# Kernel tuning notes

Measured on AMD Instinct MI355X. Metric: run time of the kernel, lower is better.

## Reference

```python
import jax, jax.numpy as jnp
import numpy as np

EPS = 1e-3  # keras LayerNormalization default epsilon


def _layernorm(y, gamma, beta):
    m = jnp.mean(y, axis=-1, keepdims=True)
    v = jnp.var(y, axis=-1, keepdims=True)
    return (y - m) * jax.lax.rsqrt(v + EPS) * gamma + beta


def setup_inputs() -> dict:
    key = jax.random.key(0)
    ks = jax.random.split(key, 3)
    B, S, D, F = 4, 8192, 512, 2048
    x = jax.random.normal(ks[0], (B, S, D), dtype=jnp.float32)
    W1 = jax.random.normal(ks[1], (D, F), dtype=jnp.float32) * (1.0 / np.sqrt(D))
    b1 = jnp.zeros((F,), dtype=jnp.float32)
    W2 = jax.random.normal(ks[2], (F, D), dtype=jnp.float32) * (1.0 / np.sqrt(F))
    b2 = jnp.zeros((D,), dtype=jnp.float32)
    g1 = jnp.ones((D,), dtype=jnp.float32)
    be1 = jnp.zeros((D,), dtype=jnp.float32)
    g2 = jnp.ones((D,), dtype=jnp.float32)
    be2 = jnp.zeros((D,), dtype=jnp.float32)
    return {"x": x, "W1": W1, "b1": b1, "W2": W2, "b2": b2,
            "g1": g1, "be1": be1, "g2": g2, "be2": be2}


def reference(x, W1, b1, W2, b2, g1, be1, g2, be2):
    # 2D FFT over (seq, embed) axes; keep real part (FNet mixing)
    fft = jnp.real(jnp.fft.fft2(x.astype(jnp.complex64), axes=(-2, -1)))
    proj_input = _layernorm(x + fft, g1, be1)
    # FFN: Dense(dense_dim, relu) -> Dense(embed_dim)
    h = jax.nn.relu(jnp.einsum('bsd,df->bsf', proj_input, W1) + b1)
    proj_output = jnp.einsum('bsf,fd->bsd', h, W2) + b2
    return _layernorm(proj_input + proj_output, g2, be2)
```

## Files before the change

kernel.cpp:

```cpp
#include <hip/hip_runtime.h>

typedef unsigned short u16;
typedef unsigned int u32;
typedef short short8 __attribute__((ext_vector_type(8)));
typedef float f32x4 __attribute__((ext_vector_type(4)));

#define LN_EPS 1e-3f
#define PI2 6.28318530717958647692f
#define AS1 __attribute__((address_space(1)))
#define AS3 __attribute__((address_space(3)))

__device__ __forceinline__ u16 f2bf(float f) {
  u32 u = __float_as_uint(f);
  u += 0x7fffu + ((u >> 16) & 1u);
  return (u16)(u >> 16);
}
__device__ __forceinline__ float bf2f(u16 h) {
  return __uint_as_float(((u32)h) << 16);
}

__global__ void prep_w(const float* __restrict__ W, u16* __restrict__ Wt, int R, int C) {
  int idx = blockIdx.x * 256 + threadIdx.x;
  int n = idx / R;
  int k = idx - n * R;
  Wt[idx] = f2bf(W[(size_t)k * C + n]);
}

__global__ __launch_bounds__(256) void transpose_x(const float* __restrict__ x,
                                                   float* __restrict__ xt) {
  __shared__ float tile[32][33];
  int blk = blockIdx.x;
  int b = blk >> 12;
  int rem = blk & 4095;
  int st = rem >> 4;
  int dt = rem & 15;
  int tx = threadIdx.x & 31, ty = threadIdx.x >> 5;
  int s0 = st << 5, d0 = dt << 5;
#pragma unroll
  for (int i = 0; i < 32; i += 8)
    tile[ty + i][tx] = x[(((size_t)(b << 13) + s0 + ty + i) << 9) + d0 + tx];
  __syncthreads();
#pragma unroll
  for (int i = 0; i < 32; i += 8)
    xt[(((size_t)(b << 9) + d0 + ty + i) << 13) + s0 + tx] = tile[tx][ty + i];
}

__device__ __constant__ float C16r[8] = {1.f, 0.92387953f, 0.70710678f, 0.38268343f,
                                         0.f, -0.38268343f, -0.70710678f, -0.92387953f};
__device__ __constant__ float C16i[8] = {0.f, -0.38268343f, -0.70710678f, -0.92387953f,
                                         -1.f, -0.92387953f, -0.70710678f, -0.38268343f};
__device__ __constant__ float C8r[4] = {1.f, 0.70710678f, 0.f, -0.70710678f};
__device__ __constant__ float C8i[4] = {0.f, -0.70710678f, -1.f, -0.70710678f};
__device__ __constant__ float C4r[2] = {1.f, 0.f};
__device__ __constant__ float C4i[2] = {0.f, -1.f};
__device__ __constant__ float C32r[16] = {
    1.f, 0.98078528f, 0.92387953f, 0.83146961f, 0.70710678f, 0.55557023f,
    0.38268343f, 0.19509032f, 0.f, -0.19509032f, -0.38268343f, -0.55557023f,
    -0.70710678f, -0.83146961f, -0.92387953f, -0.98078528f};
__device__ __constant__ float C32i[16] = {
    0.f, -0.19509032f, -0.38268343f, -0.55557023f, -0.70710678f, -0.83146961f,
    -0.92387953f, -0.98078528f, -1.f, -0.98078528f, -0.92387953f, -0.83146961f,
    -0.70710678f, -0.55557023f, -0.38268343f, -0.19509032f};
__device__ __constant__ int REV4[16] = {0, 8, 4, 12, 2, 10, 6, 14,
                                        1, 9, 5, 13, 3, 11, 7, 15};

__device__ __forceinline__ constexpr int rev4c(int v) {
  return ((v & 1) << 3) | ((v & 2) << 1) | ((v & 4) >> 1) | ((v & 8) >> 3);
}

#define BFLY(ar, ai, br, bi, wr, wi)                 \
  {                                                  \
    float dr_ = (ar) - (br), di_ = (ai) - (bi);      \
    (ar) += (br);                                    \
    (ai) += (bi);                                    \
    (br) = dr_ * (wr)-di_ * (wi);                    \
    (bi) = dr_ * (wi) + di_ * (wr);                  \
  }

__global__ __launch_bounds__(512) void fft_s(float* __restrict__ X, float* __restrict__ Xim) {
  __shared__ float zr[8448], zi[8448];
  const int t = threadIdx.x;
  const int b = blockIdx.x >> 8;
  const int d0 = (blockIdx.x & 255) << 1;
  float* r0 = X + (((size_t)(b << 9) + d0) << 13);
  float* r1 = r0 + 8192;

  float xr[16], xi[16];
#pragma unroll
  for (int e = 0; e < 16; ++e) {
    xr[e] = r0[t + (e << 9)];
    xi[e] = r1[t + (e << 9)];
  }

  float c1, s1;
  sincosf(-PI2 * (float)t * (1.0f / 8192.0f), &s1, &c1);
  float c2 = c1 * c1 - s1 * s1, s2 = 2.f * c1 * s1;
  float c4 = c2 * c2 - s2 * s2, s4 = 2.f * c2 * s2;
  float c8 = c4 * c4 - s4 * s4, s8 = 2.f * c4 * s4;
#pragma unroll
  for (int e = 0; e < 8; ++e) {
    float wr = c1 * C16r[e] - s1 * C16i[e];
    float wi = c1 * C16i[e] + s1 * C16r[e];
    BFLY(xr[e], xi[e], xr[e + 8], xi[e + 8], wr, wi);
  }
#pragma unroll
  for (int e = 0; e < 16; ++e) {
    if ((e & 4) == 0) {
      int eb = e & 3;
      float wr = c2 * C8r[eb] - s2 * C8i[eb];
      float wi = c2 * C8i[eb] + s2 * C8r[eb];
      BFLY(xr[e], xi[e], xr[e + 4], xi[e + 4], wr, wi);
    }
  }
#pragma unroll
  for (int e = 0; e < 16; ++e) {
    if (((e >> 1) & 1) == 0) {
      int eb = e & 1;
      float wr = c4 * C4r[eb] - s4 * C4i[eb];
      float wi = c4 * C4i[eb] + s4 * C4r[eb];
      BFLY(xr[e], xi[e], xr[e + 2], xi[e + 2], wr, wi);
    }
  }
#pragma unroll
  for (int e = 0; e < 16; e += 2) {
    BFLY(xr[e], xi[e], xr[e + 1], xi[e + 1], c8, s8);
  }

#pragma unroll
  for (int e = 0; e < 16; ++e) {
    int idx = t + (e << 9);
    int a = idx + (idx >> 5);
    zr[a] = xr[e];
    zi[a] = xi[e];
  }
  __syncthreads();
  {
    const int f = t >> 5, l = t & 31;
#pragma unroll
    for (int e = 0; e < 16; ++e) {
      int idx = (f << 9) + (e << 5) + l;
      int a = idx + (idx >> 5);
      xr[e] = zr[a];
      xi[e] = zi[a];
    }
    float bc1, bs1;
    sincosf(-PI2 * (float)l * (1.0f / 512.0f), &bs1, &bc1);
    float bc2 = bc1 * bc1 - bs1 * bs1, bs2 = 2.f * bc1 * bs1;
    float bc4 = bc2 * bc2 - bs2 * bs2, bs4 = 2.f * bc2 * bs2;
    float bc8 = bc4 * bc4 - bs4 * bs4, bs8 = 2.f * bc4 * bs4;
#pragma unroll
    for (int e = 0; e < 8; ++e) {
      float wr = bc1 * C16r[e] - bs1 * C16i[e];
      float wi = bc1 * C16i[e] + bs1 * C16r[e];
      BFLY(xr[e], xi[e], xr[e + 8], xi[e + 8], wr, wi);
    }
#pragma unroll
    for (int e = 0; e < 16; ++e) {
      if (((e >> 2) & 1) == 0) {
        int eb = e & 3;
        float wr = bc2 * C8r[eb] - bs2 * C8i[eb];
        float wi = bc2 * C8i[eb] + bs2 * C8r[eb];
        BFLY(xr[e], xi[e], xr[e + 4], xi[e + 4], wr, wi);
      }
    }
#pragma unroll
    for (int e = 0; e < 16; ++e) {
      if (((e >> 1) & 1) == 0) {
        int eb = e & 1;
        float wr = bc4 * C4r[eb] - bs4 * C4i[eb];
        float wi = bc4 * C4i[eb] + bs4 * C4r[eb];
        BFLY(xr[e], xi[e], xr[e + 2], xi[e + 2], wr, wi);
      }
    }
#pragma unroll
    for (int e = 0; e < 16; e += 2) {
      BFLY(xr[e], xi[e], xr[e + 1], xi[e + 1], bc8, bs8);
    }
    __syncthreads();
#pragma unroll
    for (int e = 0; e < 16; ++e) {
      int idx = (f << 9) + (e << 5) + l;
      int a = idx + (idx >> 5);
      zr[a] = xr[e];
      zi[a] = xi[e];
    }
  }
  __syncthreads();
#pragma unroll
  for (int j = 0; j < 16; ++j) {
    int idx = (t << 4) + j;
    int a = idx + (idx >> 5);
    xr[j] = zr[a];
    xi[j] = zi[a];
  }

  {
    const int odd = t & 1;
#pragma unroll
    for (int j = 0; j < 16; ++j) {
      float pr = __shfl_xor(xr[j], 1);
      float pi = __shfl_xor(xi[j], 1);
      if (!odd) {
        xr[j] += pr;
        xi[j] += pi;
      } else {
        float dr = pr - xr[j], di = pi - xi[j];
        xr[j] = dr * C32r[j] - di * C32i[j];
        xi[j] = dr * C32i[j] + di * C32r[j];
      }
    }
#pragma unroll
    for (int j = 0; j < 8; ++j) {
      BFLY(xr[j], xi[j], xr[j + 8], xi[j + 8], C16r[j], C16i[j]);
    }
#pragma unroll
    for (int j = 0; j < 16; ++j) {
      if (((j >> 2) & 1) == 0) {
        BFLY(xr[j], xi[j], xr[j + 4], xi[j + 4], C8r[j & 3], C8i[j & 3]);
      }
    }
#pragma unroll
    for (int j = 0; j < 16; ++j) {
      if (((j >> 1) & 1) == 0) {
        BFLY(xr[j], xi[j], xr[j + 2], xi[j + 2], C4r[j & 1], C4i[j & 1]);
      }
    }
#pragma unroll
    for (int j = 0; j < 16; j += 2) {
      BFLY(xr[j], xi[j], xr[j + 1], xi[j + 1], 1.0f, 0.0f);
    }
  }

  __syncthreads();
  {
    const int rt = __brev((u32)t) >> 23;
#pragma unroll
    for (int j = 0; j < 16; ++j) {
      int k = (REV4[j] << 9) | rt;
      int a = k + (k >> 5);
      zr[a] = xr[j];
      zi[a] = xi[j];
    }
  }
  __syncthreads();

  float* i0 = Xim + (((size_t)(b << 9) + d0) << 13);
  float* i1 = i0 + 8192;
#pragma unroll
  for (int e = 0; e < 16; ++e) {
    int k = t + (e << 9);
    int nk = (8192 - k) & 8191;
    int ka = k + (k >> 5), na = nk + (nk >> 5);
    float zrk = zr[ka], zik = zi[ka], zrn = zr[na], zin = zi[na];
    r0[k] = 0.5f * (zrk + zrn);
    i0[k] = 0.5f * (zik - zin);
    r1[k] = 0.5f * (zik + zin);
    i1[k] = 0.5f * (zrn - zrk);
  }
}

__global__ __launch_bounds__(256) void fft_d_ln(
    const float* __restrict__ Xre, const float* __restrict__ Xim,
    const float* __restrict__ x, const float* __restrict__ g1,
    const float* __restrict__ be1, u16* __restrict__ proj) {
  __shared__ float buf[16 * 528];
  const int tid = threadIdx.x;
  const int b = blockIdx.x >> 9;
  const int s0 = (blockIdx.x & 511) << 4;
  const int row = tid >> 4, t = tid & 15;
  const int so = tid & 15, dd = tid >> 4;

  float xr[32], xi[32];

#pragma unroll
  for (int it = 0; it < 32; ++it) {
    int d = dd + (it << 4);
    buf[so * 516 + d] = Xre[(((size_t)(b << 9) + d) << 13) + s0 + so];
  }
  __syncthreads();
#pragma unroll
  for (int e = 0; e < 32; ++e) xr[e] = buf[row * 516 + t + (e << 4)];
  __syncthreads();
#pragma unroll
  for (int it = 0; it < 32; ++it) {
    int d = dd + (it << 4);
    buf[so * 516 + d] = Xim[(((size_t)(b << 9) + d) << 13) + s0 + so];
  }
  __syncthreads();
#pragma unroll
  for (int e = 0; e < 32; ++e) xi[e] = buf[row * 516 + t + (e << 4)];
  __syncthreads();

  float c1, s1;
  sincosf(-PI2 * (float)t * (1.0f / 512.0f), &s1, &c1);
  float c2 = c1 * c1 - s1 * s1, s2 = 2.f * c1 * s1;
  float c4 = c2 * c2 - s2 * s2, s4 = 2.f * c2 * s2;
  float c8 = c4 * c4 - s4 * s4, s8 = 2.f * c4 * s4;
  float c16 = c8 * c8 - s8 * s8, s16 = 2.f * c8 * s8;
#pragma unroll
  for (int e = 0; e < 16; ++e) {
    float wr = c1 * C32r[e] - s1 * C32i[e];
    float wi = c1 * C32i[e] + s1 * C32r[e];
    BFLY(xr[e], xi[e], xr[e + 16], xi[e + 16], wr, wi);
  }
#pragma unroll
  for (int e = 0; e < 32; ++e) {
    if ((e & 8) == 0) {
      int eb = e & 7;
      float wr = c2 * C16r[eb] - s2 * C16i[eb];
      float wi = c2 * C16i[eb] + s2 * C16r[eb];
      BFLY(xr[e], xi[e], xr[e + 8], xi[e + 8], wr, wi);
    }
  }
#pragma unroll
  for (int e = 0; e < 32; ++e) {
    if ((e & 4) == 0) {
      int eb = e & 3;
      float wr = c4 * C8r[eb] - s4 * C8i[eb];
      float wi = c4 * C8i[eb] + s4 * C8r[eb];
      BFLY(xr[e], xi[e], xr[e + 4], xi[e + 4], wr, wi);
    }
  }
#pragma unroll
  for (int e = 0; e < 32; ++e) {
    if ((e & 2) == 0) {
      int eb = e & 1;
      float wr = c8 * C4r[eb] - s8 * C4i[eb];
      float wi = c8 * C4i[eb] + s8 * C4r[eb];
      BFLY(xr[e], xi[e], xr[e + 2], xi[e + 2], wr, wi);
    }
  }
#pragma unroll
  for (int e = 0; e < 32; e += 2) {
    BFLY(xr[e], xi[e], xr[e + 1], xi[e + 1], c16, s16);
  }

#pragma unroll
  for (int e = 0; e < 32; ++e) {
    int p = (e << 4) + t;
    buf[row * 528 + p + (p >> 5)] = xr[e];
  }
  __syncthreads();
#pragma unroll
  for (int j = 0; j < 32; ++j) xr[j] = buf[row * 528 + 33 * t + j];
  __syncthreads();
#pragma unroll
  for (int e = 0; e < 32; ++e) {
    int p = (e << 4) + t;
    buf[row * 528 + p + (p >> 5)] = xi[e];
  }
  __syncthreads();
#pragma unroll
  for (int j = 0; j < 32; ++j) xi[j] = buf[row * 528 + 33 * t + j];
  __syncthreads();

#pragma unroll
  for (int o = 0; o < 32; o += 16) {
#pragma unroll
    for (int j = 0; j < 8; ++j)
      BFLY(xr[o + j], xi[o + j], xr[o + j + 8], xi[o + j + 8], C16r[j], C16i[j]);
#pragma unroll
    for (int j = 0; j < 16; ++j)
      if ((j & 4) == 0)
        BFLY(xr[o + j], xi[o + j], xr[o + j + 4], xi[o + j + 4], C8r[j & 3], C8i[j & 3]);
#pragma unroll
    for (int j = 0; j < 16; ++j)
      if ((j & 2) == 0)
        BFLY(xr[o + j], xi[o + j], xr[o + j + 2], xi[o + j + 2], C4r[j & 1], C4i[j & 1]);
#pragma unroll
    for (int j = 0; j < 16; j += 2)
      BFLY(xr[o + j], xi[o + j], xr[o + j + 1], xi[o + j + 1], 1.0f, 0.0f);
  }

  {
    const int rt4 = __brev((u32)t) >> 28;
#pragma unroll
    for (int j = 0; j < 16; ++j) {
      const int rj = rev4c(j);
      buf[row * 528 + 33 * rj + rt4] = xr[j];
      buf[row * 528 + 33 * rj + 16 + rt4] = xr[16 + j];
    }
  }
  __syncthreads();

  const int s = s0 + row;
  const float* xrow = x + (((size_t)(b << 13) + s) << 9);
  float v[32];
  float sum = 0.f, sum2 = 0.f;
#pragma unroll
  for (int m = 0; m < 32; ++m) {
    int d = t + (m << 4);
    float val = buf[row * 528 + d + (d >> 5)] + xrow[d];
    v[m] = val;
    sum += val;
    sum2 += val * val;
  }
#pragma unroll
  for (int m = 1; m < 16; m <<= 1) {
    sum += __shfl_xor(sum, m, 16);
    sum2 += __shfl_xor(sum2, m, 16);
  }
  float mean = sum * (1.0f / 512.0f);
  float var = sum2 * (1.0f / 512.0f) - mean * mean;
  float scl = 1.0f / sqrtf(var + LN_EPS);
  u16* prow = proj + (((size_t)(b << 13) + s) << 9);
#pragma unroll
  for (int m = 0; m < 32; ++m) {
    int d = t + (m << 4);
    prow[d] = f2bf((v[m] - mean) * scl * g1[d] + be1[d]);
  }
}

template <bool RELU, bool OUT_BF16, int GH>
__global__ __launch_bounds__(512, 2) void gemm256(
    const u16* __restrict__ A, const u16* __restrict__ Bt,
    const float* __restrict__ bias, void* __restrict__ Cout,
    int M, int N, int K) {
  const int tid = threadIdx.x;
  const int lane = tid & 63;
  const int wave = tid >> 6;
  const int wm = wave >> 2;
  const int wn = wave & 3;
  const int llo = lane & 15, lhi = lane >> 4;

  const int nwg = gridDim.x;
  const int q = nwg >> 3;
  const int b2 = ((int)blockIdx.x & 7) * q + ((int)blockIdx.x >> 3);
  const int NT = N >> 8;
  const int GSZ = GH * NT;
  const int grp = b2 / GSZ;
  const int rr = b2 - grp * GSZ;
  const int tn = rr / GH;
  const int tm = grp * GH + (rr - tn * GH);
  const int m0 = tm << 8, n0 = tn << 8;

  __shared__ short8 smem[8192];
  char* ldsA = (char*)&smem[0];
  char* ldsB = ldsA + 65536;

  f32x4 acc[8][4] = {};

  const int trow = tid >> 3;
  const int ksw = ((tid & 7) ^ (trow & 7)) << 3;
  const int swz = (llo & 7) << 4;
  const int cb0 = (lhi << 4) ^ swz;
  const char* Ab0 = ldsA + wm * 16384 + llo * 128;
  const char* Bb0 = ldsB + (wn >> 1) * 16384 + (((wn & 1) << 6) + llo) * 128;

#define GLDS(g_, d_) __builtin_amdgcn_global_load_lds((const AS1 void*)(g_), (AS3 void*)(d_), 16, 0, 0)
#define STAGE_A(kt, hf) {                                                        \
    const u16* g_ = A + (size_t)(m0 + ((hf) << 7) + trow) * K + ((kt) << 6) + ksw; \
    char* d_ = ldsA + (((kt)&1) << 15) + ((hf) << 14) + tid * 16;                \
    GLDS(g_, d_); GLDS(g_ + ((size_t)64) * K, d_ + 8192); }
#define STAGE_B(kt, hf) {                                                        \
    const u16* g_ = Bt + (size_t)(n0 + ((hf) << 7) + trow) * K + ((kt) << 6) + ksw; \
    char* d_ = ldsB + (((kt)&1) << 15) + ((hf) << 14) + tid * 16;                \
    GLDS(g_, d_); GLDS(g_ + ((size_t)64) * K, d_ + 8192); }
#define BAR() { __builtin_amdgcn_sched_barrier(0); __builtin_amdgcn_s_barrier(); \
                __builtin_amdgcn_sched_barrier(0); }
#define VMW(n_) { asm volatile("s_waitcnt vmcnt(" #n_ ")" ::: "memory"); }

  const int KT = K >> 6;
  STAGE_A(0, 0); STAGE_A(0, 1); STAGE_B(0, 0); STAGE_B(0, 1);
  STAGE_B(1, 0); STAGE_B(1, 1);
  VMW(0);
  BAR();

  for (int t0 = 0; t0 < KT; t0 += 2) {
    const bool pf = (t0 + 2 < KT);
#pragma unroll
    for (int s = 0; s < 2; ++s) {
      const char* Abase = Ab0 + (s << 15);
      const char* Bbase = Bb0 + (s << 15);
      short8 bfr[4][2];
      {
#pragma unroll
        for (int fn = 0; fn < 4; ++fn) {
          bfr[fn][0] = *(const short8*)(Bbase + fn * 2048 + cb0);
          bfr[fn][1] = *(const short8*)(Bbase + fn * 2048 + (cb0 ^ 64));
        }
        short8 af[2][2];
#pragma unroll
        for (int i = 0; i < 2; ++i) {
          af[i][0] = *(const short8*)(Abase + i * 2048 + cb0);
          af[i][1] = *(const short8*)(Abase + i * 2048 + (cb0 ^ 64));
        }
        if (s == 0) {
          STAGE_A(t0 + 1, 0); STAGE_A(t0 + 1, 1);
        } else if (pf) {
          STAGE_A(t0 + 2, 0); STAGE_A(t0 + 2, 1);
        }
        BAR();
        __builtin_amdgcn_s_setprio(1);
#pragma unroll
        for (int i = 0; i < 2; ++i)
#pragma unroll
          for (int fn = 0; fn < 4; ++fn)
#pragma unroll
            for (int kk = 0; kk < 2; ++kk)
              acc[i][fn] = __builtin_amdgcn_mfma_f32_16x16x32_bf16(
                  af[i][kk], bfr[fn][kk], acc[i][fn], 0, 0, 0);
        __builtin_amdgcn_s_setprio(0);
        BAR();
      }
#pragma unroll
      for (int qq = 1; qq < 4; ++qq) {
        short8 af[2][2];
#pragma unroll
        for (int i = 0; i < 2; ++i) {
          af[i][0] = *(const short8*)(Abase + (qq * 2 + i) * 2048 + cb0);
          af[i][1] = *(const short8*)(Abase + (qq * 2 + i) * 2048 + (cb0 ^ 64));
        }
        if (pf) {
          if (s == 0) {
            if (qq == 1) STAGE_B(t0 + 2, 0);
            if (qq == 2) STAGE_B(t0 + 2, 1);
          } else {
            if (qq == 1) STAGE_B(t0 + 3, 0);
            if (qq == 2) STAGE_B(t0 + 3, 1);
          }
        }
        BAR();
        __builtin_amdgcn_s_setprio(1);
#pragma unroll
        for (int i = 0; i < 2; ++i)
#pragma unroll
          for (int fn = 0; fn < 4; ++fn)
#pragma unroll
            for (int kk = 0; kk < 2; ++kk)
              acc[qq * 2 + i][fn] = __builtin_amdgcn_mfma_f32_16x16x32_bf16(
                  af[i][kk], bfr[fn][kk], acc[qq * 2 + i][fn], 0, 0, 0);
        __builtin_amdgcn_s_setprio(0);
        if (qq == 3) VMW(4);
        BAR();
      }
    }
  }
#undef GLDS
#undef STAGE_A
#undef STAGE_B
#undef BAR
#undef VMW

  float bv[4];
#pragma unroll
  for (int fn = 0; fn < 4; ++fn) bv[fn] = bias[n0 + (wn << 6) + (fn << 4) + llo];
#pragma unroll
  for (int fm = 0; fm < 8; ++fm) {
#pragma unroll
    for (int j = 0; j < 4; ++j) {
      const size_t row = (size_t)(m0 + (wm << 7) + (fm << 4) + (lhi << 2) + j);
#pragma unroll
      for (int fn = 0; fn < 4; ++fn) {
        const int col = n0 + (wn << 6) + (fn << 4) + llo;
        float v = acc[fm][fn][j] + bv[fn];
        if (RELU) v = fmaxf(v, 0.0f);
        if (OUT_BF16) ((u16*)Cout)[row * N + col] = f2bf(v);
        else          ((float*)Cout)[row * N + col] = v;
      }
    }
  }
}

__global__ __launch_bounds__(256) void ln2_kernel(
    float* __restrict__ out, const u16* __restrict__ proj,
    const float* __restrict__ g2, const float* __restrict__ be2) {
  const int lane = threadIdx.x & 63;
  const int row = blockIdx.x * 4 + (threadIdx.x >> 6);
  float* orow = out + ((size_t)row << 9);
  const u16* prow = proj + ((size_t)row << 9);
  const int d0 = lane << 3;
  f32x4 a0 = *(const f32x4*)(orow + d0);
  f32x4 a1 = *(const f32x4*)(orow + d0 + 4);
  short8 p = *(const short8*)(prow + d0);
  float y[8];
  float sum = 0.f, sum2 = 0.f;
#pragma unroll
  for (int m = 0; m < 8; ++m) {
    float v = (m < 4 ? a0[m] : a1[m - 4]) + bf2f((u16)p[m]);
    y[m] = v; sum += v; sum2 += v * v;
  }
#pragma unroll
  for (int m = 1; m < 64; m <<= 1) {
    sum += __shfl_xor(sum, m, 64);
    sum2 += __shfl_xor(sum2, m, 64);
  }
  float mean = sum * (1.0f / 512.0f);
  float var = sum2 * (1.0f / 512.0f) - mean * mean;
  float scl = 1.0f / sqrtf(var + LN_EPS);
  f32x4 g0 = *(const f32x4*)(g2 + d0);
  f32x4 g1v = *(const f32x4*)(g2 + d0 + 4);
  f32x4 e0 = *(const f32x4*)(be2 + d0);
  f32x4 e1 = *(const f32x4*)(be2 + d0 + 4);
  f32x4 o0, o1;
#pragma unroll
  for (int m = 0; m < 4; ++m) o0[m] = (y[m] - mean) * scl * g0[m] + e0[m];
#pragma unroll
  for (int m = 0; m < 4; ++m) o1[m] = (y[m + 4] - mean) * scl * g1v[m] + e1[m];
  *(f32x4*)(orow + d0) = o0;
  *(f32x4*)(orow + d0 + 4) = o1;
}

extern "C" void kernel_launch(void* const* d_in, const int* in_sizes, int n_in,
                              void* d_out, int out_size, void* d_ws, size_t ws_size,
                              hipStream_t stream) {
  const float* x   = (const float*)d_in[0];
  const float* W1  = (const float*)d_in[1];
  const float* b1  = (const float*)d_in[2];
  const float* W2  = (const float*)d_in[3];
  const float* b2  = (const float*)d_in[4];
  const float* g1  = (const float*)d_in[5];
  const float* be1 = (const float*)d_in[6];
  const float* g2  = (const float*)d_in[7];
  const float* be2 = (const float*)d_in[8];

  char* ws = (char*)d_ws;
  float* xre  = (float*)(ws);
  float* xim  = (float*)(ws + (64u << 20));
  u16*   proj = (u16*)(ws + (128u << 20));
  u16*   w1t  = (u16*)(ws + (160u << 20));
  u16*   w2t  = (u16*)(ws + (162u << 20));
  u16*   h    = (u16*)(ws);

  prep_w<<<4096, 256, 0, stream>>>(W1, w1t, 512, 2048);
  prep_w<<<4096, 256, 0, stream>>>(W2, w2t, 2048, 512);
  transpose_x<<<16384, 256, 0, stream>>>(x, xre);
  fft_s<<<1024, 512, 0, stream>>>(xre, xim);
  fft_d_ln<<<2048, 256, 0, stream>>>(xre, xim, x, g1, be1, proj);
  gemm256<true, true, 4><<<1024, 512, 0, stream>>>(proj, w1t, b1, (void*)h, 32768, 2048, 512);
  gemm256<false, false, 2><<<256, 512, 0, stream>>>(h, w2t, b2, d_out, 32768, 512, 2048);
  ln2_kernel<<<8192, 256, 0, stream>>>((float*)d_out, proj, g2, be2);
  (void)in_sizes; (void)n_in; (void)out_size; (void)ws_size;
}
```

Baseline: 326.0 us.

## Use 128x128-tile GEMM for first FFN layer and tiled weight transpose

Adds a new gemm_bt kernel with 128x128 output tiles, 256 threads and single-buffered direct global-to-LDS loads, and uses it for the first FFN GEMM (K=512) instead of the 256x256 gemm256. With smaller tiles the grid grows to 4096 workgroups, which improves load balance and occupancy for the short-K GEMM, at the cost of more A/B reloading. The weight prep kernel also becomes an LDS-tiled transpose so its global reads coalesce instead of striding.

```diff
diff --git a/kernel.cpp b/kernel.cpp
--- a/kernel.cpp
+++ b/kernel.cpp
@@ -19,11 +19,21 @@
   return __uint_as_float(((u32)h) << 16);
 }
 
-__global__ void prep_w(const float* __restrict__ W, u16* __restrict__ Wt, int R, int C) {
-  int idx = blockIdx.x * 256 + threadIdx.x;
-  int n = idx / R;
-  int k = idx - n * R;
-  Wt[idx] = f2bf(W[(size_t)k * C + n]);
+__global__ __launch_bounds__(256) void prep_w(const float* __restrict__ W,
+                                              u16* __restrict__ Wt, int R, int C) {
+  __shared__ float tile[32][33];
+  const int ct = C >> 5;
+  int bc = blockIdx.x % ct;
+  int br = blockIdx.x / ct;
+  int tx = threadIdx.x & 31, ty = threadIdx.x >> 5;
+  int r0 = br << 5, c0 = bc << 5;
+#pragma unroll
+  for (int i = 0; i < 32; i += 8)
+    tile[ty + i][tx] = W[(size_t)(r0 + ty + i) * C + c0 + tx];
+  __syncthreads();
+#pragma unroll
+  for (int i = 0; i < 32; i += 8)
+    Wt[(size_t)(c0 + ty + i) * R + r0 + tx] = f2bf(tile[tx][ty + i]);
 }
 
 __global__ __launch_bounds__(256) void transpose_x(const float* __restrict__ x,
@@ -412,6 +422,90 @@
 }
 
 template <bool RELU, bool OUT_BF16, int GH>
+__global__ __launch_bounds__(256, 2) void gemm_bt(
+    const u16* __restrict__ A, const u16* __restrict__ Bt,
+    const float* __restrict__ bias, void* __restrict__ Cout,
+    int M, int N, int K) {
+  const int tid = threadIdx.x;
+  const int lane = tid & 63;
+  const int wave = tid >> 6;
+  const int wm = wave >> 1, wn = wave & 1;
+  const int llo = lane & 15, lhi = lane >> 4;
+
+  const int nwg = gridDim.x;
+  const int q = nwg >> 3;
+  const int b2 = ((int)blockIdx.x & 7) * q + ((int)blockIdx.x >> 3);
+  const int NT = N >> 7;
+  const int GSZ = GH * NT;
+  const int grp = b2 / GSZ;
+  const int r = b2 - grp * GSZ;
+  const int tn = r / GH;
+  const int tm = grp * GH + (r - tn * GH);
+  const int m0 = tm << 7, n0 = tn << 7;
+
+  __shared__ short8 smem[2048];
+  char* ldsA = (char*)&smem[0];
+  char* ldsB = ldsA + 16384;
+
+  f32x4 acc[4][4] = {};
+
+  const int trow = tid >> 3;
+  const int ksw = (((tid & 7) ^ (trow & 7)) << 3);
+  const int wbase = wave << 10;
+  const int swz = (llo & 7) << 4;
+
+  const int KT = K >> 6;
+  for (int kt = 0; kt < KT; ++kt) {
+    const int k0 = (kt << 6) + ksw;
+    __syncthreads();
+#pragma unroll
+    for (int r4 = 0; r4 < 4; ++r4) {
+      const int grow = (r4 << 5) + trow;
+      const u16* ga = A + (size_t)(m0 + grow) * K + k0;
+      const u16* gb = Bt + (size_t)(n0 + grow) * K + k0;
+      __builtin_amdgcn_global_load_lds((const AS1 void*)ga,
+                                       (AS3 void*)(ldsA + (r4 << 12) + wbase), 16, 0, 0);
+      __builtin_amdgcn_global_load_lds((const AS1 void*)gb,
+                                       (AS3 void*)(ldsB + (r4 << 12) + wbase), 16, 0, 0);
+    }
+    __syncthreads();
+#pragma unroll
+    for (int kk = 0; kk < 2; ++kk) {
+      const int cbx = ((kk << 6) | (lhi << 4)) ^ swz;
+      short8 af[4], bfr[4];
+#pragma unroll
+      for (int mt = 0; mt < 4; ++mt)
+        af[mt] = *(const short8*)(ldsA + (((wm << 6) + (mt << 4) + llo) << 7) + cbx);
+#pragma unroll
+      for (int nt = 0; nt < 4; ++nt)
+        bfr[nt] = *(const short8*)(ldsB + (((wn << 6) + (nt << 4) + llo) << 7) + cbx);
+#pragma unroll
+      for (int mt = 0; mt < 4; ++mt)
+#pragma unroll
+        for (int nt = 0; nt < 4; ++nt)
+          acc[mt][nt] =
+              __builtin_amdgcn_mfma_f32_16x16x32_bf16(af[mt], bfr[nt], acc[mt][nt], 0, 0, 0);
+    }
+  }
+#pragma unroll
+  for (int nt = 0; nt < 4; ++nt) {
+    const int col = n0 + (wn << 6) + (nt << 4) + llo;
+    const float bv = bias[col];
+#pragma unroll
+    for (int mt = 0; mt < 4; ++mt) {
+      const int rbase = m0 + (wm << 6) + (mt << 4) + (lhi << 2);
+#pragma unroll
+      for (int j = 0; j < 4; ++j) {
+        float v = acc[mt][nt][j] + bv;
+        if (RELU) v = fmaxf(v, 0.0f);
+        if (OUT_BF16) ((u16*)Cout)[(size_t)(rbase + j) * N + col] = f2bf(v);
+        else          ((float*)Cout)[(size_t)(rbase + j) * N + col] = v;
+      }
+    }
+  }
+}
+
+template <bool RELU, bool OUT_BF16, int GH>
 __global__ __launch_bounds__(512, 2) void gemm256(
     const u16* __restrict__ A, const u16* __restrict__ Bt,
     const float* __restrict__ bias, void* __restrict__ Cout,
@@ -622,12 +716,12 @@
   u16*   w2t  = (u16*)(ws + (162u << 20));
   u16*   h    = (u16*)(ws);
 
-  prep_w<<<4096, 256, 0, stream>>>(W1, w1t, 512, 2048);
-  prep_w<<<4096, 256, 0, stream>>>(W2, w2t, 2048, 512);
+  prep_w<<<1024, 256, 0, stream>>>(W1, w1t, 512, 2048);
+  prep_w<<<1024, 256, 0, stream>>>(W2, w2t, 2048, 512);
   transpose_x<<<16384, 256, 0, stream>>>(x, xre);
   fft_s<<<1024, 512, 0, stream>>>(xre, xim);
   fft_d_ln<<<2048, 256, 0, stream>>>(xre, xim, x, g1, be1, proj);
-  gemm256<true, true, 4><<<1024, 512, 0, stream>>>(proj, w1t, b1, (void*)h, 32768, 2048, 512);
+  gemm_bt<true, true, 8><<<4096, 256, 0, stream>>>(proj, w1t, b1, (void*)h, 32768, 2048, 512);
   gemm256<false, false, 2><<<256, 512, 0, stream>>>(h, w2t, b2, d_out, 32768, 512, 2048);
   ln2_kernel<<<8192, 256, 0, stream>>>((float*)d_out, proj, g2, be2);
   (void)in_sizes; (void)n_in; (void)out_size; (void)ws_size;
```

After: 316.6 us. -2.9%, faster.
